# Performance work log

Measured on AMD Instinct MI355X. Metric: run time of the kernel, lower is better.

## Reference

```python
import jax, jax.numpy as jnp
import numpy as np

B, N, F_IN, E, TOPK = 64, 1024, 64, 128, 32
NEG_SLOPE = 0.2  # GAT leaky-relu slope


def setup_inputs() -> dict:
    key = jax.random.key(0)
    ks = jax.random.split(key, 7)
    x = jax.random.normal(ks[0], (B, N, F_IN), dtype=jnp.float32)
    emb = jax.random.normal(ks[1], (N, E), dtype=jnp.float32)            # nn.Embedding table
    W_fe = jax.random.normal(ks[2], (F_IN, E), dtype=jnp.float32) / np.sqrt(F_IN).astype(np.float32)
    a_src = jax.random.normal(ks[3], (2 * E,), dtype=jnp.float32) * 0.05
    a_dst = jax.random.normal(ks[4], (2 * E,), dtype=jnp.float32) * 0.05
    lin_W = jax.random.normal(ks[5], (E, 1), dtype=jnp.float32) / np.sqrt(E).astype(np.float32)
    lin_b = jnp.zeros((1,), dtype=jnp.float32)
    return {"x": x, "emb": emb, "W_fe": W_fe, "a_src": a_src, "a_dst": a_dst,
            "lin_W": lin_W, "lin_b": lin_b}


def reference(x, emb, W_fe, a_src, a_dst, lin_W, lin_b):
    b, n, _ = x.shape
    e_dim = emb.shape[-1]
    # --- cosine-similarity topk graph construction (shared across batch) ---
    norm = jnp.linalg.norm(emb, axis=-1, keepdims=True)                  # [N,1]
    sim = (emb @ emb.T) / (norm @ norm.T)                                # [N,N]
    idx = jax.lax.top_k(sim, TOPK)[1]                                    # [N,K] int32 neighbor (target) nodes
    # --- graph attention feature extraction ---
    h = jnp.einsum('bnf,fe->bne', x, W_fe)                               # [B,N,E] projected node features
    g = jnp.concatenate([h, jnp.broadcast_to(emb, (b, n, e_dim))], -1)   # [B,N,2E] feat || embedding
    e_s = g @ a_src                                                      # [B,N] source attention term
    e_d = g @ a_dst                                                      # [B,N] target attention term
    # edges: source i repeated TOPK times -> targets idx[i]; softmax over each node's K neighbors
    scores = jax.nn.leaky_relu(e_s[:, :, None] + e_d[:, idx], NEG_SLOPE)  # [B,N,K]
    alpha = jax.nn.softmax(scores, axis=-1)                              # [B,N,K]
    h_dst = h[:, idx, :]                                                 # [B,N,K,E] gathered neighbor feats
    out = jnp.einsum('bnk,bnke->bne', alpha, h_dst)                      # aggregate messages
    out = jax.nn.relu(out)
    # --- linear readout ---
    y = out @ lin_W + lin_b                                              # [B,N,1]
    return y[..., 0]                                                     # [B,N]
```

## Files before the change

kernel.cpp:

```cpp
#include <hip/hip_runtime.h>
#include <math.h>

#define BB 64
#define NN 1024
#define F_IN 64
#define EE 128
#define TOPK 32
#define NEG_SLOPE 0.2f

typedef unsigned int uint;
typedef unsigned short ushort;
typedef unsigned long long ull;
typedef __attribute__((ext_vector_type(8))) short short8;
typedef __attribute__((ext_vector_type(4))) float f32x4;

static __device__ __forceinline__ uint f2bf(float f) {
  const uint x = __float_as_uint(f);
  return (x + 0x7fffu + ((x >> 16) & 1u)) >> 16;
}
static __device__ __forceinline__ float bf_lo(uint u) {
  return __uint_as_float(u << 16);
}
static __device__ __forceinline__ float bf_hi_raw(uint u) {
  return __uint_as_float(u);
}
static __device__ __forceinline__ uint fmono(float f) {
  uint u = __float_as_uint(f);
  return (u & 0x80000000u) ? ~u : (u | 0x80000000u);
}
static __device__ __forceinline__ ull umax64(ull a, ull b) {
  return a > b ? a : b;
}
static __device__ __forceinline__ ull umin64(ull a, ull b) {
  return a < b ? a : b;
}

__global__ __launch_bounds__(256) void k2a_sim(
    const float* __restrict__ emb, const float* __restrict__ a_src,
    const float* __restrict__ a_dst, uint* __restrict__ keys,
    float* __restrict__ u_src, float* __restrict__ u_dst) {
  __shared__ float ei[8][130];
  __shared__ float ej[64][130];
  const int t = threadIdx.x, wid = t >> 6, lane = t & 63;
  const int i0 = (blockIdx.x >> 2) * 8;
  const int jbase = (blockIdx.x & 3) * 256;

  if ((blockIdx.x & 3) == 0) {
    const int row = i0 + 2 * wid + (lane >> 5);
    const int ll = lane & 31;
    const float* er = emb + (size_t)row * EE;
    float us = 0.f, ud = 0.f;
#pragma unroll
    for (int c0 = 0; c0 < EE; c0 += 32) {
      const int c = c0 + ll;
      const float e = er[c];
      us += e * a_src[EE + c];
      ud += e * a_dst[EE + c];
    }
#pragma unroll
    for (int o = 1; o <= 16; o <<= 1) {
      us += __shfl_xor(us, o);
      ud += __shfl_xor(ud, o);
    }
    if (ll == 0) {
      u_src[row] = us;
      u_dst[row] = ud;
    }
  }

  {
    const int r = t >> 5, c4 = t & 31;
    const float4 v = *(const float4*)&emb[(size_t)(i0 + r) * EE + c4 * 4];
    *(float2*)&ei[r][c4 * 4] = make_float2(v.x, v.y);
    *(float2*)&ei[r][c4 * 4 + 2] = make_float2(v.z, v.w);
  }

  const int ia = i0 + wid * 2;

  for (int ch = 0; ch < 4; ++ch) {
    const int j0 = jbase + ch * 64;
#pragma unroll
    for (int p = 0; p < 8; ++p) {
      const int g = p * 256 + t;
      const int r = g >> 5, c4 = g & 31;
      const float4 v = *(const float4*)&emb[(size_t)(j0 + r) * EE + c4 * 4];
      *(float2*)&ej[r][c4 * 4] = make_float2(v.x, v.y);
      *(float2*)&ej[r][c4 * 4 + 2] = make_float2(v.z, v.w);
    }
    __syncthreads();

    float a0 = 0.f, a1 = 0.f, sq = 0.f;
#pragma unroll 8
    for (int d2 = 0; d2 < 64; ++d2) {
      const float2 e = *(const float2*)&ej[lane][2 * d2];
      const float2 wa = *(const float2*)&ei[wid * 2][2 * d2];
      const float2 wb = *(const float2*)&ei[wid * 2 + 1][2 * d2];
      a0 += e.x * wa.x + e.y * wa.y;
      a1 += e.x * wb.x + e.y * wb.y;
      sq += e.x * e.x + e.y * e.y;
    }
    const int jg = j0 + lane;
    const float rj = rsqrtf(sq);
    keys[(size_t)ia * NN + jg] = fmono(a0 * rj);
    keys[(size_t)(ia + 1) * NN + jg] = fmono(a1 * rj);
    __syncthreads();
  }
}

__global__ __launch_bounds__(256) void k23(
    const uint* __restrict__ keys, int* __restrict__ idx_out,
    const float* __restrict__ x, const float* __restrict__ W_fe,
    const float* __restrict__ a_src, const float* __restrict__ a_dst,
    const float* __restrict__ u_src, const float* __restrict__ u_dst,
    uint* __restrict__ h2, float* __restrict__ es, float* __restrict__ ed) {
  __shared__ __align__(16) ushort smem_w[EE * 72];
  const int t = threadIdx.x, wid = t >> 6, lane = t & 63;

  if (blockIdx.x < NN) {
    ull* cand = (ull*)smem_w;
    const int row = blockIdx.x;

    const int jb = wid * 256 + lane * 4;
    const uint4 kv = *(const uint4*)&keys[(size_t)row * NN + jb];
    ull L0 = ((ull)kv.x << 32) | (uint)(jb + 0);
    ull L1 = ((ull)kv.y << 32) | (uint)(jb + 1);
    ull L2 = ((ull)kv.z << 32) | (uint)(jb + 2);
    ull L3 = ((ull)kv.w << 32) | (uint)(jb + 3);
    {
      ull a, b;
      a = umax64(L0, L1); b = umin64(L0, L1); L0 = a; L1 = b;
      a = umax64(L2, L3); b = umin64(L2, L3); L2 = a; L3 = b;
      a = umax64(L0, L2); b = umin64(L0, L2); L0 = a; L2 = b;
      a = umax64(L1, L3); b = umin64(L1, L3); L1 = a; L3 = b;
      a = umax64(L1, L2); b = umin64(L1, L2); L1 = a; L2 = b;
    }
    for (int s = 0; s < TOPK; s++) {
      ull m = L0;
#pragma unroll
      for (int off = 32; off > 0; off >>= 1) {
        const ull o = __shfl_xor(m, off);
        m = o > m ? o : m;
      }
      if (lane == 0) cand[wid * TOPK + s] = m;
      const bool w = (L0 == m);
      L0 = w ? L1 : L0;
      L1 = w ? L2 : L1;
      L2 = w ? L3 : L2;
      L3 = w ? 0ull : L3;
    }
    __syncthreads();

    if (wid == 0) {
      ull k0 = cand[2 * lane];
      ull k1 = cand[2 * lane + 1];
#pragma unroll
      for (int k = 2; k <= 128; k <<= 1) {
#pragma unroll
        for (int d = k >> 1; d > 0; d >>= 1) {
          if (d >= 2) {
            const int pl = d >> 1;
            const ull o0 = __shfl_xor(k0, pl);
            const ull o1 = __shfl_xor(k1, pl);
            const bool keepmax =
                ((lane & (k >> 1)) == 0) == ((lane & pl) == 0);
            k0 = keepmax ? umax64(k0, o0) : umin64(k0, o0);
            k1 = keepmax ? umax64(k1, o1) : umin64(k1, o1);
          } else {
            const bool keepmax0 = ((lane & (k >> 1)) == 0);
            const ull hi = umax64(k0, k1), lo = umin64(k0, k1);
            k0 = keepmax0 ? hi : lo;
            k1 = keepmax0 ? lo : hi;
          }
        }
      }
      if (lane < 16) {
        int* ro = idx_out + (size_t)row * TOPK;
        ro[2 * lane] = (int)(k0 & 1023u);
        ro[2 * lane + 1] = (int)(k1 & 1023u);
      }
    }
  } else {
    const int row0 = (blockIdx.x - NN) * 64;

#pragma unroll
    for (int p = 0; p < 8; ++p) {
      const int idx4 = p * 256 + t;
      const int k = idx4 >> 5;
      const int n4 = (idx4 & 31) * 4;
      const float4 v = *(const float4*)&W_fe[k * EE + n4];
      smem_w[(n4 + 0) * 72 + k] = (ushort)f2bf(v.x);
      smem_w[(n4 + 1) * 72 + k] = (ushort)f2bf(v.y);
      smem_w[(n4 + 2) * 72 + k] = (ushort)f2bf(v.z);
      smem_w[(n4 + 3) * 72 + k] = (ushort)f2bf(v.w);
    }
    __syncthreads();

    const int nn = lane & 15, quad = lane >> 4;
    const int row0w = row0 + wid * 16;

    short8 af[2];
#pragma unroll
    for (int s = 0; s < 2; ++s) {
      const float* xr = x + (size_t)(row0w + nn) * F_IN + s * 32 + quad * 8;
      const float4 v0 = *(const float4*)&xr[0];
      const float4 v1 = *(const float4*)&xr[4];
      af[s][0] = (short)f2bf(v0.x);
      af[s][1] = (short)f2bf(v0.y);
      af[s][2] = (short)f2bf(v0.z);
      af[s][3] = (short)f2bf(v0.w);
      af[s][4] = (short)f2bf(v1.x);
      af[s][5] = (short)f2bf(v1.y);
      af[s][6] = (short)f2bf(v1.z);
      af[s][7] = (short)f2bf(v1.w);
    }

    f32x4 acc[8];
#pragma unroll
    for (int T = 0; T < 8; ++T) acc[T] = (f32x4){0.f, 0.f, 0.f, 0.f};

#pragma unroll
    for (int T = 0; T < 8; ++T) {
#pragma unroll
      for (int s = 0; s < 2; ++s) {
        const short8 bf =
            *(const short8*)&smem_w[(T * 16 + nn) * 72 + s * 32 + quad * 8];
        acc[T] =
            __builtin_amdgcn_mfma_f32_16x16x32_bf16(af[s], bf, acc[T], 0, 0, 0);
      }
    }

    const int growbase = row0w + quad * 4;
#pragma unroll
    for (int reg = 0; reg < 4; ++reg) {
      uint* hr = h2 + (size_t)(growbase + reg) * 64 + nn;
#pragma unroll
      for (int T4 = 0; T4 < 4; ++T4) {
        hr[T4 * 16] =
            f2bf(acc[2 * T4][reg]) | (f2bf(acc[2 * T4 + 1][reg]) << 16);
      }
    }
    float ae[8], de[8];
#pragma unroll
    for (int T = 0; T < 8; ++T) {
      ae[T] = a_src[T * 16 + nn];
      de[T] = a_dst[T * 16 + nn];
    }
#pragma unroll
    for (int reg = 0; reg < 4; ++reg) {
      float ps = 0.f, pd = 0.f;
#pragma unroll
      for (int T = 0; T < 8; ++T) {
        ps += acc[T][reg] * ae[T];
        pd += acc[T][reg] * de[T];
      }
#pragma unroll
      for (int o = 1; o <= 8; o <<= 1) {
        ps += __shfl_xor(ps, o);
        pd += __shfl_xor(pd, o);
      }
      if (nn == 0) {
        const int grow = growbase + reg;
        const int node = grow & (NN - 1);
        es[grow] = ps + u_src[node];
        ed[grow] = pd + u_dst[node];
      }
    }
  }
}

__global__ __launch_bounds__(256) void k4_attn(
    const uint* __restrict__ h2, const float* __restrict__ es,
    const float* __restrict__ ed, const int* __restrict__ idx,
    const float* __restrict__ lin_W, const float* __restrict__ lin_b,
    float* __restrict__ y) {
  const int t = threadIdx.x, wid = t >> 6, lane = t & 63;
  const int blk = blockIdx.x;
  const int xcd = blk & 7, x = blk >> 3;
  const int b = xcd * 8 + (x >> 7);
  const int half = lane >> 5, ll = lane & 31;
  const int nh = (x & 127) * 8 + wid * 2 + half;
  const int sub2 = ll >> 4, c16 = ll & 15;
  const int pbase = half * 128 + sub2 * 4;

  const float* edb = ed + (size_t)b * NN;
  const float* esb = es + (size_t)b * NN;
  const char* hb = (const char*)(h2 + (size_t)b * NN * 64);

  const int j = idx[nh * TOPK + ll];
  const int off = j << 8;
  int offk[16];
#pragma unroll
  for (int k = 0; k < 16; ++k)
    offk[k] = __builtin_amdgcn_ds_bpermute(pbase + k * 8, off);
  uint4 tv[16];
#pragma unroll
  for (int k = 0; k < 16; ++k)
    tv[k] = *(const uint4*)(hb + ((uint)offk[k] + c16 * 16));

  const float esv = esb[nh];
  float s = esv + edb[j];
  s = s > 0.f ? s : NEG_SLOPE * s;
  const float p = __expf(s);
  float dsum = p;
#pragma unroll
  for (int o = 1; o <= 16; o <<= 1) dsum += __shfl_xor(dsum, o);
  const float w = p * (1.0f / dsum);
  float wk[16];
#pragma unroll
  for (int k = 0; k < 16; ++k)
    wk[k] = __uint_as_float(
        __builtin_amdgcn_ds_bpermute(pbase + k * 8, __float_as_uint(w)));

  float lwlo[4], lwhi[4];
#pragma unroll
  for (int i = 0; i < 4; ++i) {
    const int c = 4 * c16 + i;
    const int t4 = c >> 4, nn2 = c & 15;
    lwlo[i] = lin_W[t4 * 32 + nn2];
    lwhi[i] = lin_W[t4 * 32 + 16 + nn2];
  }
  const float bias = lin_b[0];

  float acc[8];
#pragma unroll
  for (int i = 0; i < 8; i++) acc[i] = 0.f;
#pragma unroll
  for (int k = 0; k < 16; ++k) {
    const float ak = wk[k];
    const uint4 u = tv[k];
    acc[0] += ak * bf_lo(u.x);
    acc[1] += ak * bf_hi_raw(u.x);
    acc[2] += ak * bf_lo(u.y);
    acc[3] += ak * bf_hi_raw(u.y);
    acc[4] += ak * bf_lo(u.z);
    acc[5] += ak * bf_hi_raw(u.z);
    acc[6] += ak * bf_lo(u.w);
    acc[7] += ak * bf_hi_raw(u.w);
  }
#pragma unroll
  for (int i = 0; i < 8; i++) {
    acc[i] += __shfl_xor(acc[i], 16);
    acc[i] = acc[i] > 0.f ? acc[i] : 0.f;
  }
  float r = acc[0] * lwlo[0] + acc[1] * lwhi[0] + acc[2] * lwlo[1] +
            acc[3] * lwhi[1] + acc[4] * lwlo[2] + acc[5] * lwhi[2] +
            acc[6] * lwlo[3] + acc[7] * lwhi[3];
#pragma unroll
  for (int o = 8; o > 0; o >>= 1) r += __shfl_xor(r, o);
  if (ll == 0) y[(size_t)b * NN + nh] = r + bias;
}

extern "C" void kernel_launch(void* const* d_in, const int* in_sizes, int n_in,
                              void* d_out, int out_size, void* d_ws,
                              size_t ws_size, hipStream_t stream) {
  const float* x = (const float*)d_in[0];
  const float* emb = (const float*)d_in[1];
  const float* W_fe = (const float*)d_in[2];
  const float* a_src = (const float*)d_in[3];
  const float* a_dst = (const float*)d_in[4];
  const float* lin_W = (const float*)d_in[5];
  const float* lin_b = (const float*)d_in[6];
  float* y = (float*)d_out;

  char* ws = (char*)d_ws;
  float* u_src = (float*)(ws + 4096);
  float* u_dst = (float*)(ws + 8192);
  int* idx = (int*)(ws + 16384);
  float* es = (float*)(ws + 16384 + 131072);
  float* ed = (float*)(ws + 16384 + 131072 + 262144);
  uint* h2 = (uint*)(ws + 16384 + 131072 + 2 * 262144);
  uint* keys = (uint*)(ws + 16384 + 131072 + 2 * 262144 + 16777216);

  k2a_sim<<<512, 256, 0, stream>>>(emb, a_src, a_dst, keys, u_src, u_dst);
  k23<<<2048, 256, 0, stream>>>(keys, idx, x, W_fe, a_src, a_dst, u_src,
                                u_dst, h2, es, ed);
  k4_attn<<<8192, 256, 0, stream>>>(h2, es, ed, idx, lin_W, lin_b, y);
}
```

Before: 146.3 us.

## Replace iterative wave argmax top-k with full bitonic sort of per-wave keys

The per-wave top-32 selection previously ran 32 rounds of wave-wide max reductions with pop-from-sorted-list. It now bitonic-sorts all 256 packed key/index values held four per lane across the wave and takes the first 32. This aims to shorten the long serialized chain of shuffle reductions, at the cost of more compare-exchange work and more shuffles per step. A 64-bit shuffle helper built from two 32-bit shuffles is also used in the existing merge stage.

```diff
diff --git a/kernel.cpp b/kernel.cpp
--- a/kernel.cpp
+++ b/kernel.cpp
@@ -33,6 +33,11 @@
 }
 static __device__ __forceinline__ ull umin64(ull a, ull b) {
   return a < b ? a : b;
+}
+static __device__ __forceinline__ ull shfl_xor64(ull v, int mask) {
+  const uint lo = __shfl_xor((uint)v, mask);
+  const uint hi = __shfl_xor((uint)(v >> 32), mask);
+  return ((ull)hi << 32) | lo;
 }
 
 __global__ __launch_bounds__(256) void k2a_sim(
@@ -122,31 +127,51 @@
 
     const int jb = wid * 256 + lane * 4;
     const uint4 kv = *(const uint4*)&keys[(size_t)row * NN + jb];
-    ull L0 = ((ull)kv.x << 32) | (uint)(jb + 0);
-    ull L1 = ((ull)kv.y << 32) | (uint)(jb + 1);
-    ull L2 = ((ull)kv.z << 32) | (uint)(jb + 2);
-    ull L3 = ((ull)kv.w << 32) | (uint)(jb + 3);
-    {
-      ull a, b;
-      a = umax64(L0, L1); b = umin64(L0, L1); L0 = a; L1 = b;
-      a = umax64(L2, L3); b = umin64(L2, L3); L2 = a; L3 = b;
-      a = umax64(L0, L2); b = umin64(L0, L2); L0 = a; L2 = b;
-      a = umax64(L1, L3); b = umin64(L1, L3); L1 = a; L3 = b;
-      a = umax64(L1, L2); b = umin64(L1, L2); L1 = a; L2 = b;
-    }
-    for (int s = 0; s < TOPK; s++) {
-      ull m = L0;
-#pragma unroll
-      for (int off = 32; off > 0; off >>= 1) {
-        const ull o = __shfl_xor(m, off);
-        m = o > m ? o : m;
-      }
-      if (lane == 0) cand[wid * TOPK + s] = m;
-      const bool w = (L0 == m);
-      L0 = w ? L1 : L0;
-      L1 = w ? L2 : L1;
-      L2 = w ? L3 : L2;
-      L3 = w ? 0ull : L3;
+    ull xr[4];
+    xr[0] = ((ull)kv.x << 32) | (uint)(jb + 0);
+    xr[1] = ((ull)kv.y << 32) | (uint)(jb + 1);
+    xr[2] = ((ull)kv.z << 32) | (uint)(jb + 2);
+    xr[3] = ((ull)kv.w << 32) | (uint)(jb + 3);
+
+#pragma unroll
+    for (int k = 2; k <= 256; k <<= 1) {
+#pragma unroll
+      for (int d = 128; d >= 1; d >>= 1) {
+        if (d > (k >> 1)) continue;
+        if (d >= 4) {
+          const int pl = d >> 2;
+          const bool lower = (lane & pl) == 0;
+#pragma unroll
+          for (int r = 0; r < 4; ++r) {
+            const ull o = shfl_xor64(xr[r], pl);
+            const bool desc = (((lane * 4 + r) & k) == 0);
+            const bool keepmax = (desc == lower);
+            xr[r] = keepmax ? umax64(xr[r], o) : umin64(xr[r], o);
+          }
+        } else if (d == 2) {
+#pragma unroll
+          for (int r = 0; r < 2; ++r) {
+            const bool desc = (((lane * 4 + r) & k) == 0);
+            const ull hi = umax64(xr[r], xr[r + 2]);
+            const ull lo = umin64(xr[r], xr[r + 2]);
+            xr[r] = desc ? hi : lo;
+            xr[r + 2] = desc ? lo : hi;
+          }
+        } else {
+#pragma unroll
+          for (int r = 0; r < 4; r += 2) {
+            const bool desc = (((lane * 4 + r) & k) == 0);
+            const ull hi = umax64(xr[r], xr[r + 1]);
+            const ull lo = umin64(xr[r], xr[r + 1]);
+            xr[r] = desc ? hi : lo;
+            xr[r + 1] = desc ? lo : hi;
+          }
+        }
+      }
+    }
+    if (lane < 8) {
+#pragma unroll
+      for (int r = 0; r < 4; ++r) cand[wid * 32 + lane * 4 + r] = xr[r];
     }
     __syncthreads();
 
@@ -159,8 +184,8 @@
         for (int d = k >> 1; d > 0; d >>= 1) {
           if (d >= 2) {
             const int pl = d >> 1;
-            const ull o0 = __shfl_xor(k0, pl);
-            const ull o1 = __shfl_xor(k1, pl);
+            const ull o0 = shfl_xor64(k0, pl);
+            const ull o1 = shfl_xor64(k1, pl);
             const bool keepmax =
                 ((lane & (k >> 1)) == 0) == ((lane & pl) == 0);
             k0 = keepmax ? umax64(k0, o0) : umin64(k0, o0);
@@ -201,9 +226,9 @@
     short8 af[2];
 #pragma unroll
     for (int s = 0; s < 2; ++s) {
-      const float* xr = x + (size_t)(row0w + nn) * F_IN + s * 32 + quad * 8;
-      const float4 v0 = *(const float4*)&xr[0];
-      const float4 v1 = *(const float4*)&xr[4];
+      const float* xr2 = x + (size_t)(row0w + nn) * F_IN + s * 32 + quad * 8;
+      const float4 v0 = *(const float4*)&xr2[0];
+      const float4 v1 = *(const float4*)&xr2[4];
       af[s][0] = (short)f2bf(v0.x);
       af[s][1] = (short)f2bf(v0.y);
       af[s][2] = (short)f2bf(v0.z);
```

Result: faster. 139.1 us (-4.9%).
